# Kernel tuning notes

Measured on AMD Instinct MI355X. Metric: run time of the kernel, lower is better.

The kernel has to match this reference:

```python
import jax, jax.numpy as jnp
import numpy as np

N_HEADS = 16
N_CHANNELS = 1024
DIM_HEAD = N_CHANNELS // N_HEADS


def setup_inputs() -> dict:
    key = jax.random.key(0)
    k1, k2, k3, k4 = jax.random.split(key, 4)
    B, S, D = 4, 2048, N_CHANNELS
    x = jax.random.normal(k1, (B, S, D), dtype=jnp.float32)
    # in_proj: Linear(D, 3D, bias=False); torch weight shape [3D, D], y = x @ W.T
    w_in = jax.random.normal(k2, (3 * D, D), dtype=jnp.float32) * (1.0 / np.sqrt(D))
    # out_proj: Linear(D, D) with bias
    w_out = jax.random.normal(k3, (D, D), dtype=jnp.float32) * (1.0 / np.sqrt(D))
    b_out = jax.random.normal(k4, (D,), dtype=jnp.float32) * 0.01
    return {"x": x, "w_in": w_in, "w_out": w_out, "b_out": b_out}


def reference(x, w_in, w_out, b_out):
    B, S, D = x.shape
    H, Dh = N_HEADS, DIM_HEAD
    qkv = jnp.einsum('bsd,ed->bse', x, w_in)  # [B,S,3D]
    q, k, v = jnp.split(qkv, 3, axis=-1)
    # [B,S,D] -> [B,H,S,Dh]
    def to_heads(t):
        return t.reshape(B, S, H, Dh).transpose(0, 2, 1, 3)
    q, k, v = to_heads(q), to_heads(k), to_heads(v)
    scale = 1.0 / np.sqrt(Dh)
    scores = jnp.einsum('bhqd,bhkd->bhqk', q, k) * scale  # [B,H,S,S]
    attn = jax.nn.softmax(scores, axis=-1)
    out = jnp.einsum('bhqk,bhkd->bhqd', attn, v)  # [B,H,S,Dh]
    out = out.transpose(0, 2, 1, 3).reshape(B, S, D)
    return jnp.einsum('bsd,ed->bse', out, w_out) + b_out
```

## Files before the change

kernel.cpp:

```cpp
#include <hip/hip_runtime.h>

typedef __bf16 bf16;
typedef __bf16 bf16x2 __attribute__((ext_vector_type(2)));
typedef __bf16 bf16x4 __attribute__((ext_vector_type(4)));
typedef __bf16 bf16x8 __attribute__((ext_vector_type(8)));
typedef float f32x4 __attribute__((ext_vector_type(4)));

typedef __attribute__((address_space(1))) const unsigned int gq_t;
typedef __attribute__((address_space(3))) unsigned int lq_t;

__global__ __launch_bounds__(256) void cvt_bf16(const float* __restrict__ in,
                                                bf16* __restrict__ out,
                                                int n8) {
  int i = blockIdx.x * 256 + threadIdx.x;
  if (i >= n8) return;
  f32x4 a = ((const f32x4*)in)[2 * i];
  f32x4 b = ((const f32x4*)in)[2 * i + 1];
  bf16x8 o;
#pragma unroll
  for (int j = 0; j < 4; ++j) {
    o[j] = (bf16)a[j];
    o[4 + j] = (bf16)b[j];
  }
  ((bf16x8*)out)[i] = o;
}

template <typename TC, bool ADD_BIAS>
__global__ __launch_bounds__(512) void gemm_192(const bf16* __restrict__ A,
                                                const bf16* __restrict__ B,
                                                const float* __restrict__ bias,
                                                TC* __restrict__ C,
                                                int M, int N, int K, int lda) {
  __shared__ __align__(16) bf16 As[2][256 * 64];
  __shared__ __align__(16) bf16 Bs[2][192 * 64];
  const int tid = threadIdx.x;
  const int lane = tid & 63;
  const int wid = tid >> 6;
  const int wm = wid >> 2;
  const int wn = wid & 3;
  const int l16 = lane & 15;
  const int lhi = lane >> 4;
  const int lr = lane >> 3;

  const int nwg = gridDim.x * gridDim.y;
  const int bid0 = blockIdx.y * gridDim.x + blockIdx.x;
  const int swzb = (bid0 & 7) * (nwg >> 3) + (bid0 >> 3);
  const int m0 = (swzb / gridDim.x) * 256;
  const int n0 = (swzb % gridDim.x) * 192;

  const int nkt = K >> 6;

  f32x4 acc[8][3] = {};

  auto stageA = [&](int kt, int buf, int u) {
    const int chunk = wid * 4 + u;
    const int row = chunk * 8 + lr;
    const int cs = (lane & 7) ^ lr;
    const bf16* g = A + (size_t)(m0 + row) * lda + kt * 64 + cs * 8;
    __builtin_amdgcn_global_load_lds((gq_t*)g, (lq_t*)&As[buf][chunk * 512],
                                     16, 0, 0);
  };
  auto stageB = [&](int kt, int buf, int u) {
    const int chunk = wid * 3 + u;
    const int row = chunk * 8 + lr;
    const int cs = (lane & 7) ^ lr;
    const bf16* g = B + (size_t)(n0 + row) * K + kt * 64 + cs * 8;
    __builtin_amdgcn_global_load_lds((gq_t*)g, (lq_t*)&Bs[buf][chunk * 512],
                                     16, 0, 0);
  };

  stageA(0, 0, 0); stageA(0, 0, 1); stageA(0, 0, 2); stageA(0, 0, 3);
  stageB(0, 0, 0); stageB(0, 0, 1); stageB(0, 0, 2);
  asm volatile("s_waitcnt vmcnt(0)" ::: "memory");
  __builtin_amdgcn_sched_barrier(0);
  __builtin_amdgcn_s_barrier();

  for (int g = 0; g < nkt; ++g) {
    const int buf = g & 1;
    const bool donext = (g + 1) < nkt;
    const bf16* Asb = &As[buf][0];
    const bf16* Bsb = &Bs[buf][0];

    bf16x8 bfn[3][2];

#pragma unroll
    for (int q = 0; q < 4; ++q) {
      if (q == 0) {
#pragma unroll
        for (int nf = 0; nf < 3; ++nf) {
          const int nrow = wn * 48 + nf * 16 + l16;
          const int sw = nrow & 7;
#pragma unroll
          for (int ks = 0; ks < 2; ++ks) {
            const int slot = ks * 4 + lhi;
            bfn[nf][ks] =
                *(const bf16x8*)(Bsb + nrow * 64 + ((slot ^ sw) << 3));
          }
        }
      }
      bf16x8 af[2][2];
#pragma unroll
      for (int mf = 0; mf < 2; ++mf) {
        const int mrow = wm * 128 + (q * 2 + mf) * 16 + l16;
        const int sw = mrow & 7;
#pragma unroll
        for (int ks = 0; ks < 2; ++ks) {
          const int slot = ks * 4 + lhi;
          af[mf][ks] = *(const bf16x8*)(Asb + mrow * 64 + ((slot ^ sw) << 3));
        }
      }
      if (donext) {
        if (q == 0) {
          stageA(g + 1, buf ^ 1, 0);
          stageA(g + 1, buf ^ 1, 1);
          stageA(g + 1, buf ^ 1, 2);
          stageA(g + 1, buf ^ 1, 3);
        } else if (q == 1) {
          stageB(g + 1, buf ^ 1, 0);
          stageB(g + 1, buf ^ 1, 1);
          stageB(g + 1, buf ^ 1, 2);
        }
      }
      __builtin_amdgcn_s_barrier();
      asm volatile("s_waitcnt lgkmcnt(0)" ::: "memory");
      __builtin_amdgcn_sched_barrier(0);
      __builtin_amdgcn_s_setprio(1);
#pragma unroll
      for (int mf = 0; mf < 2; ++mf)
#pragma unroll
        for (int nf = 0; nf < 3; ++nf)
#pragma unroll
          for (int ks = 0; ks < 2; ++ks)
            acc[q * 2 + mf][nf] = __builtin_amdgcn_mfma_f32_16x16x32_bf16(
                af[mf][ks], bfn[nf][ks], acc[q * 2 + mf][nf], 0, 0, 0);
      __builtin_amdgcn_s_setprio(0);
      __builtin_amdgcn_s_barrier();
    }

    if (donext) {
      asm volatile("s_waitcnt vmcnt(0)" ::: "memory");
      __builtin_amdgcn_sched_barrier(0);
      __builtin_amdgcn_s_barrier();
    }
  }

#pragma unroll
  for (int i = 0; i < 8; ++i) {
    int row_base = m0 + wm * 128 + i * 16 + lhi * 4;
#pragma unroll
    for (int j = 0; j < 3; ++j) {
      int col = n0 + wn * 48 + j * 16 + l16;
      float bv = ADD_BIAS ? bias[col] : 0.0f;
#pragma unroll
      for (int r = 0; r < 4; ++r) {
        float val = acc[i][j][r] + bv;
        if constexpr (__is_same(TC, float))
          C[(size_t)(row_base + r) * N + col] = val;
        else
          C[(size_t)(row_base + r) * N + col] = (bf16)val;
      }
    }
  }
}

template <typename TC, bool ADD_BIAS>
__global__ __launch_bounds__(512) void gemm_8ph(const bf16* __restrict__ A,
                                                const bf16* __restrict__ B,
                                                const float* __restrict__ bias,
                                                TC* __restrict__ C,
                                                int M, int N, int K, int lda) {
  __shared__ __align__(16) bf16 As[3][256 * 64];
  __shared__ __align__(16) bf16 Bs[3][128 * 64];
  const int tid = threadIdx.x;
  const int lane = tid & 63;
  const int wid = tid >> 6;
  const int wm = wid >> 2;
  const int wn = wid & 3;
  const int l16 = lane & 15;
  const int lhi = lane >> 4;
  const int lr = lane >> 3;

  const int nwg = gridDim.x * gridDim.y;
  const int bid0 = blockIdx.y * gridDim.x + blockIdx.x;
  const int swzb = (bid0 & 7) * (nwg >> 3) + (bid0 >> 3);
  const int m0 = (swzb / gridDim.x) * 256;
  const int n0 = (swzb % gridDim.x) * 128;

  const int nkt = K >> 6;

  f32x4 acc[8][2] = {};

  auto stageA = [&](int kt, int buf, int u) {
    const int chunk = wid * 4 + u;
    const int row = chunk * 8 + lr;
    const int cs = (lane & 7) ^ lr;
    const bf16* g = A + (size_t)(m0 + row) * lda + kt * 64 + cs * 8;
    __builtin_amdgcn_global_load_lds((gq_t*)g, (lq_t*)&As[buf][chunk * 512],
                                     16, 0, 0);
  };
  auto stageB = [&](int kt, int buf, int u) {
    const int chunk = wid * 2 + u;
    const int row = chunk * 8 + lr;
    const int cs = (lane & 7) ^ lr;
    const bf16* g = B + (size_t)(n0 + row) * K + kt * 64 + cs * 8;
    __builtin_amdgcn_global_load_lds((gq_t*)g, (lq_t*)&Bs[buf][chunk * 512],
                                     16, 0, 0);
  };

  stageA(0, 0, 0); stageA(0, 0, 1); stageA(0, 0, 2); stageA(0, 0, 3);
  stageB(0, 0, 0); stageB(0, 0, 1);
  stageA(1, 1, 0); stageA(1, 1, 1); stageA(1, 1, 2); stageA(1, 1, 3);
  stageB(1, 1, 0); stageB(1, 1, 1);
  asm volatile("s_waitcnt vmcnt(6)" ::: "memory");
  __builtin_amdgcn_sched_barrier(0);
  __builtin_amdgcn_s_barrier();

  for (int g = 0; g < nkt; ++g) {
    const int buf = g % 3;
    const int nbuf = (g + 2) % 3;
    const bool donext = (g + 2) < nkt;
    const bf16* Asb = &As[buf][0];
    const bf16* Bsb = &Bs[buf][0];

#pragma unroll
    for (int q = 0; q < 2; ++q) {
      bf16x8 af[4][2], bfn[2][2];
#pragma unroll
      for (int mf = 0; mf < 4; ++mf) {
        const int mrow = wm * 128 + (q * 4 + mf) * 16 + l16;
        const int sw = mrow & 7;
#pragma unroll
        for (int ks = 0; ks < 2; ++ks) {
          const int slot = ks * 4 + lhi;
          af[mf][ks] = *(const bf16x8*)(Asb + mrow * 64 + ((slot ^ sw) << 3));
        }
      }
#pragma unroll
      for (int nh = 0; nh < 2; ++nh) {
        const int nrow = wn * 32 + nh * 16 + l16;
        const int sw = nrow & 7;
#pragma unroll
        for (int ks = 0; ks < 2; ++ks) {
          const int slot = ks * 4 + lhi;
          bfn[nh][ks] = *(const bf16x8*)(Bsb + nrow * 64 + ((slot ^ sw) << 3));
        }
      }
      if (donext) {
        if (q == 0) {
          stageA(g + 2, nbuf, 0);
          stageA(g + 2, nbuf, 1);
          stageA(g + 2, nbuf, 2);
        } else {
          stageA(g + 2, nbuf, 3);
          stageB(g + 2, nbuf, 0);
          stageB(g + 2, nbuf, 1);
        }
      }
      __builtin_amdgcn_s_barrier();
      asm volatile("s_waitcnt lgkmcnt(0)" ::: "memory");
      __builtin_amdgcn_sched_barrier(0);
      __builtin_amdgcn_s_setprio(1);
#pragma unroll
      for (int mf = 0; mf < 4; ++mf)
#pragma unroll
        for (int nh = 0; nh < 2; ++nh)
#pragma unroll
          for (int ks = 0; ks < 2; ++ks)
            acc[q * 4 + mf][nh] = __builtin_amdgcn_mfma_f32_16x16x32_bf16(
                af[mf][ks], bfn[nh][ks], acc[q * 4 + mf][nh], 0, 0, 0);
      __builtin_amdgcn_s_setprio(0);
      __builtin_amdgcn_s_barrier();
    }

    if (g + 1 < nkt) {
      if (donext) {
        asm volatile("s_waitcnt vmcnt(6)" ::: "memory");
      } else {
        asm volatile("s_waitcnt vmcnt(0)" ::: "memory");
      }
      __builtin_amdgcn_sched_barrier(0);
      __builtin_amdgcn_s_barrier();
    }
  }

#pragma unroll
  for (int i = 0; i < 8; ++i) {
    int row_base = m0 + wm * 128 + i * 16 + lhi * 4;
#pragma unroll
    for (int j = 0; j < 2; ++j) {
      int col = n0 + wn * 32 + j * 16 + l16;
      float bv = ADD_BIAS ? bias[col] : 0.0f;
#pragma unroll
      for (int r = 0; r < 4; ++r) {
        float val = acc[i][j][r] + bv;
        if constexpr (__is_same(TC, float))
          C[(size_t)(row_base + r) * N + col] = val;
        else
          C[(size_t)(row_base + r) * N + col] = (bf16)val;
      }
    }
  }
}

template <typename TA, typename TC, bool ADD_BIAS>
__global__ __launch_bounds__(256) void gemm_bt(const TA* __restrict__ A,
                                               const float* __restrict__ B,
                                               const float* __restrict__ bias,
                                               TC* __restrict__ C,
                                               int M, int N, int K,
                                               int lda, int row0) {
  __shared__ __align__(16) bf16 As[128][72];
  __shared__ __align__(16) bf16 Bs[128][72];
  const int tid = threadIdx.x;
  const int lane = tid & 63;
  const int wid = tid >> 6;
  const int wr = wid >> 1, wc = wid & 1;
  const int m0 = blockIdx.y * 128;
  const int n0 = blockIdx.x * 128;
  const int l16 = lane & 15;
  const int lhi = lane >> 4;

  f32x4 acc[4][4] = {};

  for (int k0 = 0; k0 < K; k0 += 64) {
    __syncthreads();
#pragma unroll
    for (int p = 0; p < 8; ++p) {
      int v = tid + p * 256;
      int row = v >> 4;
      int kc = (v & 15) * 4;
      size_t ai = (size_t)(row0 + m0 + row) * lda + k0 + kc;
      size_t bi = (size_t)(n0 + row) * K + k0 + kc;
      bf16x4 ab, bb;
      if constexpr (__is_same(TA, float)) {
        f32x4 a4 = *(const f32x4*)((const float*)A + ai);
#pragma unroll
        for (int j = 0; j < 4; ++j) ab[j] = (bf16)a4[j];
      } else {
        ab = *(const bf16x4*)((const bf16*)A + ai);
      }
      f32x4 b4 = *(const f32x4*)(B + bi);
#pragma unroll
      for (int j = 0; j < 4; ++j) bb[j] = (bf16)b4[j];
      *(bf16x4*)(&As[row][kc]) = ab;
      *(bf16x4*)(&Bs[row][kc]) = bb;
    }
    __syncthreads();
#pragma unroll
    for (int ks = 0; ks < 2; ++ks) {
      bf16x8 af[4], bfr[4];
#pragma unroll
      for (int i = 0; i < 4; ++i) {
        af[i] = *(const bf16x8*)(&As[wr * 64 + i * 16 + l16][ks * 32 + lhi * 8]);
        bfr[i] = *(const bf16x8*)(&Bs[wc * 64 + i * 16 + l16][ks * 32 + lhi * 8]);
      }
#pragma unroll
      for (int i = 0; i < 4; ++i)
#pragma unroll
        for (int j = 0; j < 4; ++j)
          acc[i][j] = __builtin_amdgcn_mfma_f32_16x16x32_bf16(af[i], bfr[j],
                                                              acc[i][j], 0, 0, 0);
    }
  }

#pragma unroll
  for (int i = 0; i < 4; ++i) {
    int row_base = m0 + wr * 64 + i * 16 + lhi * 4;
#pragma unroll
    for (int j = 0; j < 4; ++j) {
      int col = n0 + wc * 64 + j * 16 + l16;
      float bv = ADD_BIAS ? bias[col] : 0.0f;
#pragma unroll
      for (int r = 0; r < 4; ++r) {
        float val = acc[i][j][r] + bv;
        if constexpr (__is_same(TC, float))
          C[(size_t)(row_base + r) * N + col] = val;
        else
          C[(size_t)(row_base + r) * N + col] = (bf16)val;
      }
    }
  }
}

__global__ __launch_bounds__(512) void attn_fwd(bf16* __restrict__ qkv) {
  constexpr int S = 2048, D3 = 3072;
  constexpr float SCL = 0.18033688011112042f;
  constexpr float THR = 11.5f;
  __shared__ __align__(16) bf16 Kt[2][64][72];
  __shared__ __align__(16) bf16 Vt[2][64][72];
  __shared__ __align__(16) bf16 Pq[8][16][72];

  const int tid = threadIdx.x;
  const int lane = tid & 63;
  const int wid = tid >> 6;
  const int l16 = lane & 15, lhi = lane >> 4;

  const int nwg = gridDim.x * gridDim.y;
  const int bid = blockIdx.y * gridDim.x + blockIdx.x;
  const int swz = (bid & 7) * (nwg >> 3) + (bid >> 3);
  const int bh = swz >> 3;
  const int b = bh >> 4, h = bh & 15;
  const int q0 = (swz & 7) * 256 + wid * 32;

  bf16* base = qkv + (size_t)b * S * D3;
  bf16* qbase = base + h * 64;
  const bf16* kbase = base + 1024 + h * 64;
  const bf16* vbase = base + 2048 + h * 64;

  bf16x8 qfA[2], qfB[2];
#pragma unroll
  for (int ks = 0; ks < 2; ++ks) {
    qfA[ks] = *(const bf16x8*)(qbase + (size_t)(q0 + l16) * D3 + ks * 32 + lhi * 8);
    qfB[ks] = *(const bf16x8*)(qbase + (size_t)(q0 + 16 + l16) * D3 + ks * 32 + lhi * 8);
  }

  float mA = -1e30f, mB = -1e30f;
  float lA = 0.0f, lB = 0.0f;
  f32x4 oA[4] = {}, oB[4] = {};

  const int sg = tid >> 8;
  const int kp = tid & 31;
  const int oc = (tid >> 5) & 7;

  const bf16* sbase = (sg == 0) ? kbase : vbase;

  {
    bf16x8 s0 = *(const bf16x8*)(sbase + (size_t)(2 * kp) * D3 + oc * 8);
    bf16x8 s1 = *(const bf16x8*)(sbase + (size_t)(2 * kp + 1) * D3 + oc * 8);
    if (sg == 0) {
      *(bf16x8*)(&Kt[0][2 * kp][oc * 8]) = s0;
      *(bf16x8*)(&Kt[0][2 * kp + 1][oc * 8]) = s1;
    } else {
#pragma unroll
      for (int j = 0; j < 8; ++j) {
        bf16x2 pr;
        pr[0] = s0[j];
        pr[1] = s1[j];
        *(bf16x2*)(&Vt[0][oc * 8 + j][2 * kp]) = pr;
      }
    }
  }
  __syncthreads();

  for (int t = 0; t < S; t += 64) {
    const int cur = (t >> 6) & 1;
    const bool havenext = (t + 64 < S);

    bf16x8 n0r, n1r;
    if (havenext) {
      const bf16* sb = sbase + (size_t)(t + 64) * D3;
      n0r = *(const bf16x8*)(sb + (size_t)(2 * kp) * D3 + oc * 8);
      n1r = *(const bf16x8*)(sb + (size_t)(2 * kp + 1) * D3 + oc * 8);
    }

    f32x4 scA[4] = {}, scB[4] = {};
    __builtin_amdgcn_s_setprio(1);
#pragma unroll
    for (int ct = 0; ct < 4; ++ct) {
#pragma unroll
      for (int ks = 0; ks < 2; ++ks) {
        bf16x8 kf = *(const bf16x8*)(&Kt[cur][ct * 16 + l16][ks * 32 + lhi * 8]);
        scA[ct] = __builtin_amdgcn_mfma_f32_16x16x32_bf16(kf, qfA[ks], scA[ct], 0, 0, 0);
        scB[ct] = __builtin_amdgcn_mfma_f32_16x16x32_bf16(kf, qfB[ks], scB[ct], 0, 0, 0);
      }
    }
    __builtin_amdgcn_s_setprio(0);

    {
      float cm[4];
#pragma unroll
      for (int ct = 0; ct < 4; ++ct)
        cm[ct] = fmaxf(fmaxf(scA[ct][0], scA[ct][1]), fmaxf(scA[ct][2], scA[ct][3]));
      float mxs = fmaxf(fmaxf(cm[0], cm[1]), fmaxf(cm[2], cm[3])) * SCL;
      if (!__all(mxs - mA <= THR)) {
        float mw = mxs;
        mw = fmaxf(mw, __shfl_xor(mw, 16));
        mw = fmaxf(mw, __shfl_xor(mw, 32));
        float nm = fmaxf(mA, mw);
        float alpha = __builtin_amdgcn_exp2f(mA - nm);
        mA = nm;
        lA *= alpha;
#pragma unroll
        for (int dt = 0; dt < 4; ++dt)
#pragma unroll
          for (int r = 0; r < 4; ++r) oA[dt][r] *= alpha;
      }
      float rs4[4];
#pragma unroll
      for (int ct = 0; ct < 4; ++ct) {
#pragma unroll
        for (int r = 0; r < 4; ++r) {
          float p = __builtin_amdgcn_exp2f(__builtin_fmaf(scA[ct][r], SCL, -mA));
          scA[ct][r] = p;
        }
        rs4[ct] = (scA[ct][0] + scA[ct][1]) + (scA[ct][2] + scA[ct][3]);
      }
      lA += (rs4[0] + rs4[1]) + (rs4[2] + rs4[3]);
    }
#pragma unroll
    for (int ct = 0; ct < 4; ++ct) {
      bf16x4 pk;
#pragma unroll
      for (int r = 0; r < 4; ++r) pk[r] = (bf16)scA[ct][r];
      *(bf16x4*)(&Pq[wid][l16][ct * 16 + lhi * 4]) = pk;
    }
    bf16x8 pfA0 = *(const bf16x8*)(&Pq[wid][l16][lhi * 8]);
    bf16x8 pfA1 = *(const bf16x8*)(&Pq[wid][l16][32 + lhi * 8]);

    {
      float cm[4];
#pragma unroll
      for (int ct = 0; ct < 4; ++ct)
        cm[ct] = fmaxf(fmaxf(scB[ct][0], scB[ct][1]), fmaxf(scB[ct][2], scB[ct][3]));
      float mxs = fmaxf(fmaxf(cm[0], cm[1]), fmaxf(cm[2], cm[3])) * SCL;
      if (!__all(mxs - mB <= THR)) {
        float mw = mxs;
        mw = fmaxf(mw, __shfl_xor(mw, 16));
        mw = fmaxf(mw, __shfl_xor(mw, 32));
        float nm = fmaxf(mB, mw);
        float alpha = __builtin_amdgcn_exp2f(mB - nm);
        mB = nm;
        lB *= alpha;
#pragma unroll
        for (int dt = 0; dt < 4; ++dt)
#pragma unroll
          for (int r = 0; r < 4; ++r) oB[dt][r] *= alpha;
      }
      float rs4[4];
#pragma unroll
      for (int ct = 0; ct < 4; ++ct) {
#pragma unroll
        for (int r = 0; r < 4; ++r) {
          float p = __builtin_amdgcn_exp2f(__builtin_fmaf(scB[ct][r], SCL, -mB));
          scB[ct][r] = p;
        }
        rs4[ct] = (scB[ct][0] + scB[ct][1]) + (scB[ct][2] + scB[ct][3]);
      }
      lB += (rs4[0] + rs4[1]) + (rs4[2] + rs4[3]);
    }
#pragma unroll
    for (int ct = 0; ct < 4; ++ct) {
      bf16x4 pk;
#pragma unroll
      for (int r = 0; r < 4; ++r) pk[r] = (bf16)scB[ct][r];
      *(bf16x4*)(&Pq[wid][l16][ct * 16 + lhi * 4]) = pk;
    }
    bf16x8 pfB0 = *(const bf16x8*)(&Pq[wid][l16][lhi * 8]);
    bf16x8 pfB1 = *(const bf16x8*)(&Pq[wid][l16][32 + lhi * 8]);

    if (havenext) {
      if (sg == 0) {
        *(bf16x8*)(&Kt[cur ^ 1][2 * kp][oc * 8]) = n0r;
        *(bf16x8*)(&Kt[cur ^ 1][2 * kp + 1][oc * 8]) = n1r;
      } else {
#pragma unroll
        for (int j = 0; j < 8; ++j) {
          bf16x2 pr;
          pr[0] = n0r[j];
          pr[1] = n1r[j];
          *(bf16x2*)(&Vt[cur ^ 1][oc * 8 + j][2 * kp]) = pr;
        }
      }
    }

    __builtin_amdgcn_s_setprio(1);
#pragma unroll
    for (int dt = 0; dt < 4; ++dt) {
      bf16x8 vf0 = *(const bf16x8*)(&Vt[cur][dt * 16 + l16][lhi * 8]);
      bf16x8 vf1 = *(const bf16x8*)(&Vt[cur][dt * 16 + l16][32 + lhi * 8]);
      oA[dt] = __builtin_amdgcn_mfma_f32_16x16x32_bf16(vf0, pfA0, oA[dt], 0, 0, 0);
      oA[dt] = __builtin_amdgcn_mfma_f32_16x16x32_bf16(vf1, pfA1, oA[dt], 0, 0, 0);
      oB[dt] = __builtin_amdgcn_mfma_f32_16x16x32_bf16(vf0, pfB0, oB[dt], 0, 0, 0);
      oB[dt] = __builtin_amdgcn_mfma_f32_16x16x32_bf16(vf1, pfB1, oB[dt], 0, 0, 0);
    }
    __builtin_amdgcn_s_setprio(0);

    __syncthreads();
  }

  {
    float l_i = lA;
    l_i += __shfl_xor(l_i, 16);
    l_i += __shfl_xor(l_i, 32);
    float rl = 1.0f / l_i;
#pragma unroll
    for (int dt = 0; dt < 4; ++dt) {
      bf16x4 ok;
#pragma unroll
      for (int r = 0; r < 4; ++r) ok[r] = (bf16)(oA[dt][r] * rl);
      *(bf16x4*)(&Pq[wid][l16][dt * 16 + lhi * 4]) = ok;
    }
    bf16x8 r0 = *(const bf16x8*)(&Pq[wid][l16][lhi * 16]);
    bf16x8 r1 = *(const bf16x8*)(&Pq[wid][l16][lhi * 16 + 8]);
    bf16* orow = qbase + (size_t)(q0 + l16) * D3 + lhi * 16;
    *(bf16x8*)(orow) = r0;
    *(bf16x8*)(orow + 8) = r1;
  }
  {
    float l_i = lB;
    l_i += __shfl_xor(l_i, 16);
    l_i += __shfl_xor(l_i, 32);
    float rl = 1.0f / l_i;
#pragma unroll
    for (int dt = 0; dt < 4; ++dt) {
      bf16x4 ok;
#pragma unroll
      for (int r = 0; r < 4; ++r) ok[r] = (bf16)(oB[dt][r] * rl);
      *(bf16x4*)(&Pq[wid][l16][dt * 16 + lhi * 4]) = ok;
    }
    bf16x8 r0 = *(const bf16x8*)(&Pq[wid][l16][lhi * 16]);
    bf16x8 r1 = *(const bf16x8*)(&Pq[wid][l16][lhi * 16 + 8]);
    bf16* orow = qbase + (size_t)(q0 + 16 + l16) * D3 + lhi * 16;
    *(bf16x8*)(orow) = r0;
    *(bf16x8*)(orow + 8) = r1;
  }
}

extern "C" void kernel_launch(void* const* d_in, const int* in_sizes, int n_in,
                              void* d_out, int out_size, void* d_ws,
                              size_t ws_size, hipStream_t stream) {
  constexpr int B = 4, S = 2048, D = 1024;

  const float* x = nullptr;
  const float* w_in = nullptr;
  const float* w_out = nullptr;
  const float* b_out = nullptr;
  for (int i = 0; i < n_in; ++i) {
    switch (in_sizes[i]) {
      case 8388608: x = (const float*)d_in[i]; break;
      case 3145728: w_in = (const float*)d_in[i]; break;
      case 1048576: w_out = (const float*)d_in[i]; break;
      case 1024: b_out = (const float*)d_in[i]; break;
    }
  }
  float* out = (float*)d_out;

  bf16* qkv = (bf16*)d_ws;
  const size_t need_full = (size_t)B * S * 3 * D * 2;
  const size_t need_cvt = need_full +
                          ((size_t)B * S * D +
                           (size_t)3 * D * D +
                           (size_t)D * D) * 2;

  if (ws_size >= need_cvt) {
    bf16* xb = qkv + (size_t)B * S * 3 * D;
    bf16* w_inb = xb + (size_t)B * S * D;
    bf16* w_outb = w_inb + (size_t)3 * D * D;
    const int nx8 = B * S * D / 8;
    const int nwi8 = 3 * D * D / 8;
    const int nwo8 = D * D / 8;
    cvt_bf16<<<dim3((nx8 + 255) / 256), 256, 0, stream>>>(x, xb, nx8);
    cvt_bf16<<<dim3((nwi8 + 255) / 256), 256, 0, stream>>>(w_in, w_inb, nwi8);
    cvt_bf16<<<dim3((nwo8 + 255) / 256), 256, 0, stream>>>(w_out, w_outb, nwo8);

    gemm_192<bf16, false><<<dim3(3 * D / 192, B * S / 256), 512, 0, stream>>>(
        xb, w_inb, nullptr, qkv, B * S, 3 * D, D, D);
    attn_fwd<<<dim3(S / 256, B * 16), 512, 0, stream>>>(qkv);
    gemm_8ph<float, true><<<dim3(D / 128, B * S / 256), 512, 0, stream>>>(
        qkv, w_outb, b_out, out, B * S, D, D, 3 * D);
  } else if (ws_size >= need_full) {
    gemm_bt<float, bf16, false><<<dim3(3 * D / 128, B * S / 128), 256, 0,
                                  stream>>>(x, w_in, nullptr, qkv, B * S,
                                            3 * D, D, D, 0);
    attn_fwd<<<dim3(S / 256, B * 16), 512, 0, stream>>>(qkv);
    gemm_bt<bf16, float, true><<<dim3(D / 128, B * S / 128), 256, 0, stream>>>(
        qkv, w_out, b_out, out, B * S, D, D, 3 * D, 0);
  } else {
    for (int b0 = 0; b0 < B; ++b0) {
      gemm_bt<float, bf16, false><<<dim3(3 * D / 128, S / 128), 256, 0,
                                    stream>>>(x, w_in, nullptr, qkv, S, 3 * D,
                                              D, D, b0 * S);
      attn_fwd<<<dim3(S / 256, 16), 512, 0, stream>>>(qkv);
      gemm_bt<bf16, float, true><<<dim3(D / 128, S / 128), 256, 0, stream>>>(
          qkv, w_out, b_out, out + (size_t)b0 * S * D, S, D, D, 3 * D, 0);
    }
  }
}
```

Measured before the change: 288.0 us.

## Halve attention query tile per wave and single-buffer K/V in shared memory

Each wave of the attention kernel now handles 16 query rows instead of 32, so the grid doubles to S/128 blocks per head. The K/V shared tiles drop from double to single buffering: the next K tile is stored after a barrier that follows the QK^T MMAs, and the next V tile after the barrier that follows the PV MMAs. This lowers registers and LDS per block and raises parallelism, at the cost of loading each K/V tile twice as often per query and adding a second barrier per iteration.

```diff
diff --git a/kernel.cpp b/kernel.cpp
--- a/kernel.cpp
+++ b/kernel.cpp
@@ -386,8 +386,8 @@
   constexpr int S = 2048, D3 = 3072;
   constexpr float SCL = 0.18033688011112042f;
   constexpr float THR = 11.5f;
-  __shared__ __align__(16) bf16 Kt[2][64][72];
-  __shared__ __align__(16) bf16 Vt[2][64][72];
+  __shared__ __align__(16) bf16 Kt[64][72];
+  __shared__ __align__(16) bf16 Vt[64][72];
   __shared__ __align__(16) bf16 Pq[8][16][72];
 
   const int tid = threadIdx.x;
@@ -398,25 +398,23 @@
   const int nwg = gridDim.x * gridDim.y;
   const int bid = blockIdx.y * gridDim.x + blockIdx.x;
   const int swz = (bid & 7) * (nwg >> 3) + (bid >> 3);
-  const int bh = swz >> 3;
+  const int bh = swz >> 4;
   const int b = bh >> 4, h = bh & 15;
-  const int q0 = (swz & 7) * 256 + wid * 32;
+  const int q0 = (swz & 15) * 128 + wid * 16;
 
   bf16* base = qkv + (size_t)b * S * D3;
   bf16* qbase = base + h * 64;
   const bf16* kbase = base + 1024 + h * 64;
   const bf16* vbase = base + 2048 + h * 64;
 
-  bf16x8 qfA[2], qfB[2];
-#pragma unroll
-  for (int ks = 0; ks < 2; ++ks) {
-    qfA[ks] = *(const bf16x8*)(qbase + (size_t)(q0 + l16) * D3 + ks * 32 + lhi * 8);
-    qfB[ks] = *(const bf16x8*)(qbase + (size_t)(q0 + 16 + l16) * D3 + ks * 32 + lhi * 8);
-  }
-
-  float mA = -1e30f, mB = -1e30f;
-  float lA = 0.0f, lB = 0.0f;
-  f32x4 oA[4] = {}, oB[4] = {};
+  bf16x8 qf[2];
+#pragma unroll
+  for (int ks = 0; ks < 2; ++ks)
+    qf[ks] = *(const bf16x8*)(qbase + (size_t)(q0 + l16) * D3 + ks * 32 + lhi * 8);
+
+  float m_i = -1e30f;
+  float l_p = 0.0f;
+  f32x4 o[4] = {};
 
   const int sg = tid >> 8;
   const int kp = tid & 31;
@@ -428,22 +426,21 @@
     bf16x8 s0 = *(const bf16x8*)(sbase + (size_t)(2 * kp) * D3 + oc * 8);
     bf16x8 s1 = *(const bf16x8*)(sbase + (size_t)(2 * kp + 1) * D3 + oc * 8);
     if (sg == 0) {
-      *(bf16x8*)(&Kt[0][2 * kp][oc * 8]) = s0;
-      *(bf16x8*)(&Kt[0][2 * kp + 1][oc * 8]) = s1;
+      *(bf16x8*)(&Kt[2 * kp][oc * 8]) = s0;
+      *(bf16x8*)(&Kt[2 * kp + 1][oc * 8]) = s1;
     } else {
 #pragma unroll
       for (int j = 0; j < 8; ++j) {
         bf16x2 pr;
         pr[0] = s0[j];
         pr[1] = s1[j];
-        *(bf16x2*)(&Vt[0][oc * 8 + j][2 * kp]) = pr;
+        *(bf16x2*)(&Vt[oc * 8 + j][2 * kp]) = pr;
       }
     }
   }
   __syncthreads();
 
   for (int t = 0; t < S; t += 64) {
-    const int cur = (t >> 6) & 1;
     const bool havenext = (t + 64 < S);
 
     bf16x8 n0r, n1r;
@@ -453,133 +450,90 @@
       n1r = *(const bf16x8*)(sb + (size_t)(2 * kp + 1) * D3 + oc * 8);
     }
 
-    f32x4 scA[4] = {}, scB[4] = {};
+    f32x4 sc[4] = {};
     __builtin_amdgcn_s_setprio(1);
 #pragma unroll
     for (int ct = 0; ct < 4; ++ct) {
 #pragma unroll
       for (int ks = 0; ks < 2; ++ks) {
-        bf16x8 kf = *(const bf16x8*)(&Kt[cur][ct * 16 + l16][ks * 32 + lhi * 8]);
-        scA[ct] = __builtin_amdgcn_mfma_f32_16x16x32_bf16(kf, qfA[ks], scA[ct], 0, 0, 0);
-        scB[ct] = __builtin_amdgcn_mfma_f32_16x16x32_bf16(kf, qfB[ks], scB[ct], 0, 0, 0);
+        bf16x8 kf = *(const bf16x8*)(&Kt[ct * 16 + l16][ks * 32 + lhi * 8]);
+        sc[ct] = __builtin_amdgcn_mfma_f32_16x16x32_bf16(kf, qf[ks], sc[ct], 0, 0, 0);
       }
     }
     __builtin_amdgcn_s_setprio(0);
+
+    __syncthreads();
+    if (havenext && sg == 0) {
+      *(bf16x8*)(&Kt[2 * kp][oc * 8]) = n0r;
+      *(bf16x8*)(&Kt[2 * kp + 1][oc * 8]) = n1r;
+    }
 
     {
       float cm[4];
 #pragma unroll
       for (int ct = 0; ct < 4; ++ct)
-        cm[ct] = fmaxf(fmaxf(scA[ct][0], scA[ct][1]), fmaxf(scA[ct][2], scA[ct][3]));
+        cm[ct] = fmaxf(fmaxf(sc[ct][0], sc[ct][1]), fmaxf(sc[ct][2], sc[ct][3]));
       float mxs = fmaxf(fmaxf(cm[0], cm[1]), fmaxf(cm[2], cm[3])) * SCL;
-      if (!__all(mxs - mA <= THR)) {
+      if (!__all(mxs - m_i <= THR)) {
         float mw = mxs;
         mw = fmaxf(mw, __shfl_xor(mw, 16));
         mw = fmaxf(mw, __shfl_xor(mw, 32));
-        float nm = fmaxf(mA, mw);
-        float alpha = __builtin_amdgcn_exp2f(mA - nm);
-        mA = nm;
-        lA *= alpha;
+        float nm = fmaxf(m_i, mw);
+        float alpha = __builtin_amdgcn_exp2f(m_i - nm);
+        m_i = nm;
+        l_p *= alpha;
 #pragma unroll
         for (int dt = 0; dt < 4; ++dt)
 #pragma unroll
-          for (int r = 0; r < 4; ++r) oA[dt][r] *= alpha;
+          for (int r = 0; r < 4; ++r) o[dt][r] *= alpha;
       }
       float rs4[4];
 #pragma unroll
       for (int ct = 0; ct < 4; ++ct) {
 #pragma unroll
         for (int r = 0; r < 4; ++r) {
-          float p = __builtin_amdgcn_exp2f(__builtin_fmaf(scA[ct][r], SCL, -mA));
-          scA[ct][r] = p;
+          float p = __builtin_amdgcn_exp2f(__builtin_fmaf(sc[ct][r], SCL, -m_i));
+          sc[ct][r] = p;
         }
-        rs4[ct] = (scA[ct][0] + scA[ct][1]) + (scA[ct][2] + scA[ct][3]);
-      }
-      lA += (rs4[0] + rs4[1]) + (rs4[2] + rs4[3]);
-    }
+        rs4[ct] = (sc[ct][0] + sc[ct][1]) + (sc[ct][2] + sc[ct][3]);
+      }
+      l_p += (rs4[0] + rs4[1]) + (rs4[2] + rs4[3]);
+    }
+
 #pragma unroll
     for (int ct = 0; ct < 4; ++ct) {
       bf16x4 pk;
 #pragma unroll
-      for (int r = 0; r < 4; ++r) pk[r] = (bf16)scA[ct][r];
+      for (int r = 0; r < 4; ++r) pk[r] = (bf16)sc[ct][r];
       *(bf16x4*)(&Pq[wid][l16][ct * 16 + lhi * 4]) = pk;
     }
-    bf16x8 pfA0 = *(const bf16x8*)(&Pq[wid][l16][lhi * 8]);
-    bf16x8 pfA1 = *(const bf16x8*)(&Pq[wid][l16][32 + lhi * 8]);
-
-    {
-      float cm[4];
-#pragma unroll
-      for (int ct = 0; ct < 4; ++ct)
-        cm[ct] = fmaxf(fmaxf(scB[ct][0], scB[ct][1]), fmaxf(scB[ct][2], scB[ct][3]));
-      float mxs = fmaxf(fmaxf(cm[0], cm[1]), fmaxf(cm[2], cm[3])) * SCL;
-      if (!__all(mxs - mB <= THR)) {
-        float mw = mxs;
-        mw = fmaxf(mw, __shfl_xor(mw, 16));
-        mw = fmaxf(mw, __shfl_xor(mw, 32));
-        float nm = fmaxf(mB, mw);
-        float alpha = __builtin_amdgcn_exp2f(mB - nm);
-        mB = nm;
-        lB *= alpha;
-#pragma unroll
-        for (int dt = 0; dt < 4; ++dt)
-#pragma unroll
-          for (int r = 0; r < 4; ++r) oB[dt][r] *= alpha;
-      }
-      float rs4[4];
-#pragma unroll
-      for (int ct = 0; ct < 4; ++ct) {
-#pragma unroll
-        for (int r = 0; r < 4; ++r) {
-          float p = __builtin_amdgcn_exp2f(__builtin_fmaf(scB[ct][r], SCL, -mB));
-          scB[ct][r] = p;
-        }
-        rs4[ct] = (scB[ct][0] + scB[ct][1]) + (scB[ct][2] + scB[ct][3]);
-      }
-      lB += (rs4[0] + rs4[1]) + (rs4[2] + rs4[3]);
-    }
-#pragma unroll
-    for (int ct = 0; ct < 4; ++ct) {
-      bf16x4 pk;
-#pragma unroll
-      for (int r = 0; r < 4; ++r) pk[r] = (bf16)scB[ct][r];
-      *(bf16x4*)(&Pq[wid][l16][ct * 16 + lhi * 4]) = pk;
-    }
-    bf16x8 pfB0 = *(const bf16x8*)(&Pq[wid][l16][lhi * 8]);
-    bf16x8 pfB1 = *(const bf16x8*)(&Pq[wid][l16][32 + lhi * 8]);
-
-    if (havenext) {
-      if (sg == 0) {
-        *(bf16x8*)(&Kt[cur ^ 1][2 * kp][oc * 8]) = n0r;
-        *(bf16x8*)(&Kt[cur ^ 1][2 * kp + 1][oc * 8]) = n1r;
-      } else {
-#pragma unroll
-        for (int j = 0; j < 8; ++j) {
-          bf16x2 pr;
-          pr[0] = n0r[j];
-          pr[1] = n1r[j];
-          *(bf16x2*)(&Vt[cur ^ 1][oc * 8 + j][2 * kp]) = pr;
-        }
-      }
-    }
+    bf16x8 pf0 = *(const bf16x8*)(&Pq[wid][l16][lhi * 8]);
+    bf16x8 pf1 = *(const bf16x8*)(&Pq[wid][l16][32 + lhi * 8]);
 
     __builtin_amdgcn_s_setprio(1);
 #pragma unroll
     for (int dt = 0; dt < 4; ++dt) {
-      bf16x8 vf0 = *(const bf16x8*)(&Vt[cur][dt * 16 + l16][lhi * 8]);
-      bf16x8 vf1 = *(const bf16x8*)(&Vt[cur][dt * 16 + l16][32 + lhi * 8]);
-      oA[dt] = __builtin_amdgcn_mfma_f32_16x16x32_bf16(vf0, pfA0, oA[dt], 0, 0, 0);
-      oA[dt] = __builtin_amdgcn_mfma_f32_16x16x32_bf16(vf1, pfA1, oA[dt], 0, 0, 0);
-      oB[dt] = __builtin_amdgcn_mfma_f32_16x16x32_bf16(vf0, pfB0, oB[dt], 0, 0, 0);
-      oB[dt] = __builtin_amdgcn_mfma_f32_16x16x32_bf16(vf1, pfB1, oB[dt], 0, 0, 0);
+      bf16x8 vf0 = *(const bf16x8*)(&Vt[dt * 16 + l16][lhi * 8]);
+      bf16x8 vf1 = *(const bf16x8*)(&Vt[dt * 16 + l16][32 + lhi * 8]);
+      o[dt] = __builtin_amdgcn_mfma_f32_16x16x32_bf16(vf0, pf0, o[dt], 0, 0, 0);
+      o[dt] = __builtin_amdgcn_mfma_f32_16x16x32_bf16(vf1, pf1, o[dt], 0, 0, 0);
     }
     __builtin_amdgcn_s_setprio(0);
 
     __syncthreads();
+    if (havenext && sg == 1) {
+#pragma unroll
+      for (int j = 0; j < 8; ++j) {
+        bf16x2 pr;
+        pr[0] = n0r[j];
+        pr[1] = n1r[j];
+        *(bf16x2*)(&Vt[oc * 8 + j][2 * kp]) = pr;
+      }
+    }
   }
 
   {
-    float l_i = lA;
+    float l_i = l_p;
     l_i += __shfl_xor(l_i, 16);
     l_i += __shfl_xor(l_i, 32);
     float rl = 1.0f / l_i;
@@ -587,30 +541,12 @@
     for (int dt = 0; dt < 4; ++dt) {
       bf16x4 ok;
 #pragma unroll
-      for (int r = 0; r < 4; ++r) ok[r] = (bf16)(oA[dt][r] * rl);
+      for (int r = 0; r < 4; ++r) ok[r] = (bf16)(o[dt][r] * rl);
       *(bf16x4*)(&Pq[wid][l16][dt * 16 + lhi * 4]) = ok;
     }
     bf16x8 r0 = *(const bf16x8*)(&Pq[wid][l16][lhi * 16]);
     bf16x8 r1 = *(const bf16x8*)(&Pq[wid][l16][lhi * 16 + 8]);
     bf16* orow = qbase + (size_t)(q0 + l16) * D3 + lhi * 16;
-    *(bf16x8*)(orow) = r0;
-    *(bf16x8*)(orow + 8) = r1;
-  }
-  {
-    float l_i = lB;
-    l_i += __shfl_xor(l_i, 16);
-    l_i += __shfl_xor(l_i, 32);
-    float rl = 1.0f / l_i;
-#pragma unroll
-    for (int dt = 0; dt < 4; ++dt) {
-      bf16x4 ok;
-#pragma unroll
-      for (int r = 0; r < 4; ++r) ok[r] = (bf16)(oB[dt][r] * rl);
-      *(bf16x4*)(&Pq[wid][l16][dt * 16 + lhi * 4]) = ok;
-    }
-    bf16x8 r0 = *(const bf16x8*)(&Pq[wid][l16][lhi * 16]);
-    bf16x8 r1 = *(const bf16x8*)(&Pq[wid][l16][lhi * 16 + 8]);
-    bf16* orow = qbase + (size_t)(q0 + 16 + l16) * D3 + lhi * 16;
     *(bf16x8*)(orow) = r0;
     *(bf16x8*)(orow + 8) = r1;
   }
@@ -655,14 +591,14 @@
 
     gemm_192<bf16, false><<<dim3(3 * D / 192, B * S / 256), 512, 0, stream>>>(
         xb, w_inb, nullptr, qkv, B * S, 3 * D, D, D);
-    attn_fwd<<<dim3(S / 256, B * 16), 512, 0, stream>>>(qkv);
+    attn_fwd<<<dim3(S / 128, B * 16), 512, 0, stream>>>(qkv);
     gemm_8ph<float, true><<<dim3(D / 128, B * S / 256), 512, 0, stream>>>(
         qkv, w_outb, b_out, out, B * S, D, D, 3 * D);
   } else if (ws_size >= need_full) {
     gemm_bt<float, bf16, false><<<dim3(3 * D / 128, B * S / 128), 256, 0,
                                   stream>>>(x, w_in, nullptr, qkv, B * S,
                                             3 * D, D, D, 0);
-    attn_fwd<<<dim3(S / 256, B * 16), 512, 0, stream>>>(qkv);
+    attn_fwd<<<dim3(S / 128, B * 16), 512, 0, stream>>>(qkv);
     gemm_bt<bf16, float, true><<<dim3(D / 128, B * S / 128), 256, 0, stream>>>(
         qkv, w_out, b_out, out, B * S, D, D, 3 * D, 0);
   } else {
@@ -670,7 +606,7 @@
       gemm_bt<float, bf16, false><<<dim3(3 * D / 128, S / 128), 256, 0,
                                     stream>>>(x, w_in, nullptr, qkv, S, 3 * D,
                                               D, D, b0 * S);
-      attn_fwd<<<dim3(S / 256, 16), 512, 0, stream>>>(qkv);
+      attn_fwd<<<dim3(S / 128, 16), 512, 0, stream>>>(qkv);
       gemm_bt<bf16, float, true><<<dim3(D / 128, S / 128), 256, 0, stream>>>(
           qkv, w_out, b_out, out + (size_t)b0 * S * D, S, D, D, 3 * D, 0);
     }
```

Result: slower. 297.4 us (+3.2%).
